# Performance work log

Hardware: AMD Instinct MI355X
Metric: run time of the kernel (lower is better)

Reference implementation:

```python
import jax, jax.numpy as jnp
import numpy as np

B, N, CI, CP, H, W, R = 2, 8192, 64, 64, 128, 128, 4
D = (CI + CP) // R  # qk channels = 32
BN_EPS = 1e-5


def setup_inputs() -> dict:
    key = jax.random.key(0)
    ks = jax.random.split(key, 8)
    pts_img = jax.random.uniform(ks[0], (B, N, 2), minval=-1.0, maxval=1.0)
    img_feats = jax.random.normal(ks[1], (B, CI, H, W), dtype=jnp.float32)
    pts_feats = jax.random.normal(ks[2], (B, CP, N), dtype=jnp.float32)
    qk_w = jax.random.normal(ks[3], (D, CI + CP), dtype=jnp.float32) * 0.05
    v_w = jax.random.normal(ks[4], (CP, CP), dtype=jnp.float32) * 0.05
    v_b = jnp.zeros((CP,), dtype=jnp.float32)
    t_w = jax.random.normal(ks[5], (CP, CP), dtype=jnp.float32) * 0.05
    t_b = jnp.zeros((CP,), dtype=jnp.float32)
    bn_gamma = jnp.ones((CP,), dtype=jnp.float32)
    bn_beta = jnp.zeros((CP,), dtype=jnp.float32)
    return dict(pts_img=pts_img, img_feats=img_feats, pts_feats=pts_feats,
                qk_w=qk_w, v_w=v_w, v_b=v_b, t_w=t_w, t_b=t_b,
                bn_gamma=bn_gamma, bn_beta=bn_beta)


def _grid_sample(img_feats, pts_img):
    # torch.nn.functional.grid_sample: bilinear, zeros padding, align_corners=False
    # img_feats [B,C,H,W], pts_img [B,N,2] with (x,y) in [-1,1] -> [B,C,N]
    ix = (pts_img[..., 0] + 1.0) * 0.5 * W - 0.5
    iy = (pts_img[..., 1] + 1.0) * 0.5 * H - 0.5
    x0 = jnp.floor(ix); y0 = jnp.floor(iy)
    x1 = x0 + 1.0;      y1 = y0 + 1.0
    wx1 = ix - x0; wx0 = 1.0 - wx1
    wy1 = iy - y0; wy0 = 1.0 - wy1

    def gather(imgb, yi, xi):  # imgb [C,H,W]; yi,xi [N] float corner coords
        valid = ((xi >= 0) & (xi <= W - 1) & (yi >= 0) & (yi <= H - 1)).astype(imgb.dtype)
        xc = jnp.clip(xi, 0, W - 1).astype(jnp.int32)
        yc = jnp.clip(yi, 0, H - 1).astype(jnp.int32)
        return imgb[:, yc, xc] * valid  # [C,N], zeros outside

    def per_batch(imgb, x0, x1, y0, y1, wx0, wx1, wy0, wy1):
        return (gather(imgb, y0, x0) * (wy0 * wx0) + gather(imgb, y0, x1) * (wy0 * wx1)
                + gather(imgb, y1, x0) * (wy1 * wx0) + gather(imgb, y1, x1) * (wy1 * wx1))

    return jax.vmap(per_batch)(img_feats, x0, x1, y0, y1, wx0, wx1, wy0, wy1)


def reference(pts_img, img_feats, pts_feats, qk_w, v_w, v_b, t_w, t_b, bn_gamma, bn_beta):
    # grid-sample image features at point projections, concat with point features
    pts_wise_img = _grid_sample(img_feats, pts_img)                 # [B,CI,N]
    fusion = jnp.concatenate([pts_wise_img, pts_feats], axis=1)     # [B,CI+CP,N]

    # shared-weight 1x1 conv Q/K (bias=False), V with bias
    x_q = jnp.einsum('dc,bcn->bnd', qk_w, fusion)                   # [B,N,D]
    x_k = jnp.einsum('dc,bcn->bdn', qk_w, fusion)                   # [B,D,N]
    x_v = jnp.einsum('oc,bcn->bon', v_w, pts_feats) + v_b[None, :, None]  # [B,CP,N]

    energy = jnp.einsum('bnd,bdm->bnm', x_q, x_k)                   # [B,N,N]
    attention = jax.nn.softmax(energy, axis=-1)
    # L1 renormalization over rows (dim=1): divide each column by its column-sum
    attention = attention / (1e-9 + attention.sum(axis=1, keepdims=True))

    x_r = jnp.einsum('bcn,bnm->bcm', x_v, attention)                # [B,CP,N]

    # trans_conv(pts_feats - x_r) -> BatchNorm1d (training stats) -> ReLU
    y = jnp.einsum('oc,bcn->bon', t_w, pts_feats - x_r) + t_b[None, :, None]
    mean = y.mean(axis=(0, 2), keepdims=True)
    var = y.var(axis=(0, 2), keepdims=True)  # biased, matching torch BN
    y = (y - mean) * jax.lax.rsqrt(var + BN_EPS)
    y = y * bn_gamma[None, :, None] + bn_beta[None, :, None]
    x_r_out = jax.nn.relu(y)

    return pts_feats + x_r_out
```

## Files before the change

### kernel.cpp

```cpp
#include <hip/hip_runtime.h>
#include <math.h>

#define BB 2
#define NN 8192
#define CI 64
#define CP 64
#define HH 128
#define WW 128
#define DD 32
#define CF 128
#define SPLITM 8
#define SPLITN 4

typedef __bf16 bf16_t;
typedef __bf16 bf16x8 __attribute__((ext_vector_type(8)));
typedef __bf16 bf16x4 __attribute__((ext_vector_type(4)));
typedef float f32x4 __attribute__((ext_vector_type(4)));

#define SQ_L2E 1.2011224087864498f

__device__ __forceinline__ float fexp2(float x) { return __builtin_amdgcn_exp2f(x); }

__device__ __forceinline__ bf16x8 pack8(float a0,float a1,float a2,float a3,
                                        float b0,float b1,float b2,float b3){
    bf16x8 r;
    r[0]=(bf16_t)a0; r[1]=(bf16_t)a1; r[2]=(bf16_t)a2; r[3]=(bf16_t)a3;
    r[4]=(bf16_t)b0; r[5]=(bf16_t)b1; r[6]=(bf16_t)b2; r[7]=(bf16_t)b3;
    return r;
}

__device__ __forceinline__ bf16x8 ld_av(const bf16_t* p){
    bf16x4 lo = *(const bf16x4*)p;
    bf16x4 hi = *(const bf16x4*)(p + 16);
    bf16x8 r;
    r[0]=lo[0];r[1]=lo[1];r[2]=lo[2];r[3]=lo[3];
    r[4]=hi[0];r[5]=hi[1];r[6]=hi[2];r[7]=hi[3];
    return r;
}

__device__ __forceinline__ void gload_lds16(const void* g, void* l) {
    __builtin_amdgcn_global_load_lds(
        (const __attribute__((address_space(1))) unsigned int*)g,
        (__attribute__((address_space(3))) unsigned int*)l, 16, 0, 0);
}

__global__ __launch_bounds__(256) void k_timg(const float* __restrict__ img, float* __restrict__ imgT) {
    __shared__ float tile[64][65];
    int b = blockIdx.y;
    int pos0 = blockIdx.x * 64;
    int tid = threadIdx.x;
    int q = tid >> 6, r = tid & 63;
    const float* src = img + (size_t)b * CI * (HH * WW);
#pragma unroll
    for (int cc = 0; cc < 16; ++cc) {
        int c = cc * 4 + q;
        tile[c][r] = src[(size_t)c * (HH * WW) + pos0 + r];
    }
    __syncthreads();
    float* dst = imgT + ((size_t)b * (HH * WW) + pos0) * 64;
#pragma unroll
    for (int pp = 0; pp < 16; ++pp) {
        int pos = pp * 4 + q;
        dst[(size_t)pos * 64 + r] = tile[r][pos];
    }
}

__global__ __launch_bounds__(256) void k_fuse(
    const float* __restrict__ pts_img, const float* __restrict__ imgT,
    const float* __restrict__ pfeat, const float* __restrict__ qkw,
    const float* __restrict__ vw, const float* __restrict__ vb,
    bf16_t* __restrict__ Qb, bf16_t* __restrict__ XVb)
{
    __shared__ __align__(16) float qk_l[DD * 132];
    __shared__ __align__(16) float vw_l[CP * 68];
    __shared__ __align__(16) float fus[16][CF];
    __shared__ bf16_t xvout[64][20];
    int tid = threadIdx.x;
    for (int i = tid; i < DD * CF; i += 256) qk_l[(i >> 7) * 132 + (i & 127)] = qkw[i];
    for (int i = tid; i < CP * CP; i += 256) vw_l[(i >> 6) * 68 + (i & 63)] = vw[i];

    int w = tid >> 6, l = tid & 63;
    int p0 = blockIdx.x * 16;
    int bb = p0 / NN, n0 = p0 % NN;

#pragma unroll
    for (int i = 0; i < 4; ++i) {
        int pt = i * 4 + w;
        int n = n0 + pt;
        float x = pts_img[(size_t)(p0 + pt) * 2 + 0];
        float y = pts_img[(size_t)(p0 + pt) * 2 + 1];
        float ix = (x + 1.f) * 0.5f * WW - 0.5f;
        float iy = (y + 1.f) * 0.5f * HH - 0.5f;
        float x0 = floorf(ix), y0 = floorf(iy);
        float wx1 = ix - x0, wx0 = 1.f - wx1;
        float wy1 = iy - y0, wy0 = 1.f - wy1;
        int xi0 = (int)x0, yi0 = (int)y0;
        const float* base = imgT + (size_t)bb * (HH * WW) * 64 + l;
        float iv = 0.f;
#pragma unroll
        for (int cr = 0; cr < 4; ++cr) {
            int xi = xi0 + (cr & 1), yi = yi0 + (cr >> 1);
            float wgt = ((cr & 1) ? wx1 : wx0) * ((cr >> 1) ? wy1 : wy0);
            bool v = (xi >= 0) & (xi <= WW - 1) & (yi >= 0) & (yi <= HH - 1);
            int cx = min(max(xi, 0), WW - 1), cy = min(max(yi, 0), HH - 1);
            float s = base[((size_t)cy * WW + cx) * 64];
            iv += (v ? s : 0.f) * wgt;
        }
        float pv = pfeat[((size_t)bb * CP + l) * NN + n];
        fus[pt][l] = iv;
        fus[pt][64 + l] = pv;
    }
    __syncthreads();
#pragma unroll
    for (int i = 0; i < 4; ++i) {
        int pt = i * 4 + w;
        int n = n0 + pt;
        {
            int qo = l & 31, kh = l >> 5;
            const float4* qr = (const float4*)&qk_l[qo * 132 + kh * 64];
            const float4* fp = (const float4*)&fus[pt][kh * 64];
            float acc = 0.f;
#pragma unroll
            for (int k = 0; k < 16; ++k) {
                float4 a = qr[k], bq = fp[k];
                acc += a.x * bq.x + a.y * bq.y + a.z * bq.z + a.w * bq.w;
            }
            acc += __shfl_xor(acc, 32);
            if (kh == 0) Qb[((size_t)bb * NN + n) * DD + qo] = (bf16_t)(acc * SQ_L2E);
        }
        {
            const float4* vr = (const float4*)&vw_l[l * 68];
            const float4* fp = (const float4*)&fus[pt][64];
            float acc = vb[l];
#pragma unroll
            for (int k = 0; k < 16; ++k) {
                float4 a = vr[k], bv = fp[k];
                acc += a.x * bv.x + a.y * bv.y + a.z * bv.z + a.w * bv.w;
            }
            xvout[l][pt] = (bf16_t)acc;
        }
    }
    __syncthreads();
    {
        int c = tid >> 2, seg = (tid & 3) * 4;
        bf16x4 vv;
        vv[0] = xvout[c][seg + 0];
        vv[1] = xvout[c][seg + 1];
        vv[2] = xvout[c][seg + 2];
        vv[3] = xvout[c][seg + 3];
        *(bf16x4*)&XVb[((size_t)bb * CP + c) * NN + n0 + seg] = vv;
    }
}

__global__ __launch_bounds__(256) void k_rowsum(
    const bf16_t* __restrict__ Qb, float* __restrict__ rowsumG)
{
    int b = blockIdx.z;
    int n0 = blockIdx.x * 64;
    int mchunk = blockIdx.y * (NN / SPLITM);
    int tid = threadIdx.x;
    int wv = tid >> 6, l = tid & 63;
    int g = l >> 4, c16 = l & 15;
    const bf16x8* Qv = (const bf16x8*)(Qb + (size_t)b * NN * DD);
    f32x4 z = {0.f, 0.f, 0.f, 0.f};

    bf16x8 A0 = Qv[(size_t)(n0 +  0 + c16) * 4 + g];
    bf16x8 A1 = Qv[(size_t)(n0 + 16 + c16) * 4 + g];
    bf16x8 A2 = Qv[(size_t)(n0 + 32 + c16) * 4 + g];
    bf16x8 A3 = Qv[(size_t)(n0 + 48 + c16) * 4 + g];

    float rs[4][4];
#pragma unroll
    for (int a = 0; a < 4; ++a)
#pragma unroll
        for (int r = 0; r < 4; ++r) rs[a][r] = 0.f;

    int mbase = mchunk + wv * 64;
    bf16x8 Bn0 = Qv[(size_t)(mbase +  0 + c16) * 4 + g];
    bf16x8 Bn1 = Qv[(size_t)(mbase + 16 + c16) * 4 + g];
    bf16x8 Bn2 = Qv[(size_t)(mbase + 32 + c16) * 4 + g];
    bf16x8 Bn3 = Qv[(size_t)(mbase + 48 + c16) * 4 + g];

    const int NIT = NN / SPLITM / 256;
    for (int it = 0; it < NIT; ++it) {
        bf16x8 B0 = Bn0, B1 = Bn1, B2 = Bn2, B3 = Bn3;
        int mnext = mbase + 256;
        if (it + 1 < NIT) {
            Bn0 = Qv[(size_t)(mnext +  0 + c16) * 4 + g];
            Bn1 = Qv[(size_t)(mnext + 16 + c16) * 4 + g];
            Bn2 = Qv[(size_t)(mnext + 32 + c16) * 4 + g];
            Bn3 = Qv[(size_t)(mnext + 48 + c16) * 4 + g];
        }
#define ROWSTEP(Aa, a)                                                        \
        {                                                                     \
            f32x4 e0 = __builtin_amdgcn_mfma_f32_16x16x32_bf16(Aa, B0, z, 0, 0, 0); \
            f32x4 e1 = __builtin_amdgcn_mfma_f32_16x16x32_bf16(Aa, B1, z, 0, 0, 0); \
            f32x4 e2 = __builtin_amdgcn_mfma_f32_16x16x32_bf16(Aa, B2, z, 0, 0, 0); \
            f32x4 e3 = __builtin_amdgcn_mfma_f32_16x16x32_bf16(Aa, B3, z, 0, 0, 0); \
            _Pragma("unroll")                                                 \
            for (int r = 0; r < 4; ++r)                                       \
                rs[a][r] += (fexp2(e0[r]) + fexp2(e1[r])) + (fexp2(e2[r]) + fexp2(e3[r])); \
        }
        ROWSTEP(A0, 0) ROWSTEP(A1, 1) ROWSTEP(A2, 2) ROWSTEP(A3, 3)
#undef ROWSTEP
        mbase = mnext;
    }
#pragma unroll
    for (int a = 0; a < 4; ++a)
#pragma unroll
        for (int r = 0; r < 4; ++r) {
            float v = rs[a][r];
            v += __shfl_xor(v, 1);
            v += __shfl_xor(v, 2);
            v += __shfl_xor(v, 4);
            v += __shfl_xor(v, 8);
            if (c16 == 0)
                atomicAdd(&rowsumG[(size_t)b * NN + n0 + 16 * a + 4 * g + r], v);
        }
}

__global__ __launch_bounds__(256) void k_scale(
    const float* __restrict__ rowsumG, const bf16_t* __restrict__ XVb,
    bf16_t* __restrict__ XVs, bf16_t* __restrict__ irsb)
{
    int b = blockIdx.y;
    int cq = blockIdx.z;
    int n = (blockIdx.x * 256 + threadIdx.x) * 4;
    float4 rs = *(const float4*)&rowsumG[(size_t)b * NN + n];
    float ir0 = 1.f / rs.x, ir1 = 1.f / rs.y, ir2 = 1.f / rs.z, ir3 = 1.f / rs.w;
    if (cq == 0) {
        bf16x4 iv;
        iv[0] = (bf16_t)ir0; iv[1] = (bf16_t)ir1; iv[2] = (bf16_t)ir2; iv[3] = (bf16_t)ir3;
        *(bf16x4*)&irsb[(size_t)b * NN + n] = iv;
    }
    const bf16_t* src = XVb + ((size_t)b * CP + cq * 16) * NN + n;
    char* dstbase = (char*)(XVs + ((size_t)b * CP + cq * 16) * NN);
    size_t nb = (size_t)n * 2;
    size_t hi = nb & ~(size_t)255;
    size_t lo = nb & 255;
#pragma unroll
    for (int c = 0; c < 16; ++c) {
        bf16x4 v = *(const bf16x4*)&src[(size_t)c * NN];
        bf16x4 o;
        o[0] = (bf16_t)((float)v[0] * ir0);
        o[1] = (bf16_t)((float)v[1] * ir1);
        o[2] = (bf16_t)((float)v[2] * ir2);
        o[3] = (bf16_t)((float)v[3] * ir3);
        size_t sb = hi | (lo ^ ((size_t)(c & 7) << 4));
        *(bf16x4*)(dstbase + (size_t)c * NN * 2 + sb) = o;
    }
}

__device__ __forceinline__ void stage_tile(const char* xvbase, int n0, char* ldsbuf, int wv, int l) {
#pragma unroll
    for (int k = 0; k < 2; ++k) {
        int R0 = k * 32 + wv * 4;
        int row = R0 + (l >> 4);
        const char* g = xvbase + (size_t)row * (NN * 2) + (size_t)n0 * 2 + (size_t)(l & 15) * 16;
        gload_lds16(g, ldsbuf + R0 * 256);
    }
}

__global__ __launch_bounds__(512, 4) void k_attn(
    const bf16_t* __restrict__ Qb, const bf16_t* __restrict__ XVs,
    const bf16_t* __restrict__ irsb,
    bf16_t* __restrict__ part, float* __restrict__ cpart)
{
    __shared__ __align__(16) char lds[4 * 64 * 72 * 2];
    __shared__ float csL[4 * 64];

    int b = blockIdx.z;
    int m0 = blockIdx.x * 64;
    int chunk = blockIdx.y;
    int tid = threadIdx.x;
    int wv = tid >> 6, l = tid & 63;
    int g = l >> 4, c16 = l & 15;
    int q4 = wv & 3;
    int jh = wv >> 2;

    const bf16x8* Qv = (const bf16x8*)(Qb + (size_t)b * NN * DD);
    const char* xvbase = (const char*)(XVs + (size_t)b * CP * NN);
    const bf16_t* irow = irsb + (size_t)b * NN;

    bf16x8 bqA = Qv[(size_t)(m0 + jh * 32 + c16) * 4 + g];
    bf16x8 bqB = Qv[(size_t)(m0 + jh * 32 + 16 + c16) * 4 + g];

    f32x4 z = {0.f, 0.f, 0.f, 0.f};
    f32x4 acc[4][2];
    f32x4 acsA = z, acsB = z;
#pragma unroll
    for (int ci = 0; ci < 4; ++ci) { acc[ci][0] = z; acc[ci][1] = z; }

    const int NT = (NN / SPLITN) / 128;
    int nbase = chunk * (NN / SPLITN);

    stage_tile(xvbase, nbase, lds, wv, l);
    int nwin = nbase + q4 * 32;
    bf16x8 a0 = Qv[(size_t)(nwin + c16) * 4 + g];
    bf16x8 a1 = Qv[(size_t)(nwin + 16 + c16) * 4 + g];
    bf16x8 cif = ld_av(irow + nwin + 4 * g);
    __syncthreads();

    const int swz = (c16 & 7) << 4;
    const int blo = (q4 * 32 + 4 * g) * 2;
    const int lo_off = blo ^ swz;
    const int hi_off = (blo + 32) ^ swz;

    for (int t = 0; t < NT; ++t) {
        char* buf = lds + (t & 1) * 16384;
        if (t + 1 < NT)
            stage_tile(xvbase, nbase + (t + 1) * 128, lds + ((t + 1) & 1) * 16384, wv, l);

        bf16x8 ca0 = a0, ca1 = a1, cf = cif;

        f32x4 EA0 = __builtin_amdgcn_mfma_f32_16x16x32_bf16(ca0, bqA, z, 0, 0, 0);
        f32x4 EA1 = __builtin_amdgcn_mfma_f32_16x16x32_bf16(ca1, bqA, z, 0, 0, 0);
        f32x4 EB0 = __builtin_amdgcn_mfma_f32_16x16x32_bf16(ca0, bqB, z, 0, 0, 0);
        f32x4 EB1 = __builtin_amdgcn_mfma_f32_16x16x32_bf16(ca1, bqB, z, 0, 0, 0);

        bf16x8 bpA = pack8(fexp2(EA0[0]), fexp2(EA0[1]), fexp2(EA0[2]), fexp2(EA0[3]),
                           fexp2(EA1[0]), fexp2(EA1[1]), fexp2(EA1[2]), fexp2(EA1[3]));
        bf16x8 bpB = pack8(fexp2(EB0[0]), fexp2(EB0[1]), fexp2(EB0[2]), fexp2(EB0[3]),
                           fexp2(EB1[0]), fexp2(EB1[1]), fexp2(EB1[2]), fexp2(EB1[3]));

        acsA = __builtin_amdgcn_mfma_f32_16x16x32_bf16(cf, bpA, acsA, 0, 0, 0);
        acsB = __builtin_amdgcn_mfma_f32_16x16x32_bf16(cf, bpB, acsB, 0, 0, 0);

#pragma unroll
        for (int ci = 0; ci < 4; ++ci) {
            const char* rp = buf + (16 * ci + c16) * 256;
            bf16x4 lo = *(const bf16x4*)(rp + lo_off);
            bf16x4 hi = *(const bf16x4*)(rp + hi_off);
            bf16x8 xv;
            xv[0]=lo[0];xv[1]=lo[1];xv[2]=lo[2];xv[3]=lo[3];
            xv[4]=hi[0];xv[5]=hi[1];xv[6]=hi[2];xv[7]=hi[3];
            acc[ci][0] = __builtin_amdgcn_mfma_f32_16x16x32_bf16(xv, bpA, acc[ci][0], 0, 0, 0);
            acc[ci][1] = __builtin_amdgcn_mfma_f32_16x16x32_bf16(xv, bpB, acc[ci][1], 0, 0, 0);
        }

        if (t + 1 < NT) {
            int nw2 = nbase + (t + 1) * 128 + q4 * 32;
            a0 = Qv[(size_t)(nw2 + c16) * 4 + g];
            a1 = Qv[(size_t)(nw2 + 16 + c16) * 4 + g];
            cif = ld_av(irow + nw2 + 4 * g);
        }
        __syncthreads();
    }

    if (l < 16) {
        csL[q4 * 64 + 16 * (2 * jh + 0) + l] = acsA[0];
        csL[q4 * 64 + 16 * (2 * jh + 1) + l] = acsB[0];
    }
    bf16_t* epi = (bf16_t*)lds;
#pragma unroll
    for (int ci = 0; ci < 4; ++ci)
#pragma unroll
        for (int jj = 0; jj < 2; ++jj)
#pragma unroll
            for (int r = 0; r < 4; ++r) {
                int cc = 16 * ci + 4 * g + r;
                int mm = jh * 32 + jj * 16 + c16;
                epi[((size_t)q4 * 64 + cc) * 72 + mm] = (bf16_t)acc[ci][jj][r];
            }
    __syncthreads();
    {
        int c = tid >> 3, m8 = (tid & 7) * 8;
        float s[8] = {0.f,0.f,0.f,0.f,0.f,0.f,0.f,0.f};
#pragma unroll
        for (int q = 0; q < 4; ++q) {
            bf16x8 v = *(const bf16x8*)&epi[((size_t)q * 64 + c) * 72 + m8];
#pragma unroll
            for (int i = 0; i < 8; ++i) s[i] += (float)v[i];
        }
        bf16x8 o;
#pragma unroll
        for (int i = 0; i < 8; ++i) o[i] = (bf16_t)s[i];
        *(bf16x8*)&part[(((size_t)chunk * BB + b) * CP + c) * NN + m0 + m8] = o;
    }
    if (tid < 64) {
        float cp = csL[tid] + csL[64 + tid] + csL[128 + tid] + csL[192 + tid];
        cpart[((size_t)chunk * BB + b) * NN + m0 + tid] = cp;
    }
}

__global__ __launch_bounds__(256) void k_post(
    const bf16_t* __restrict__ part, const float* __restrict__ cpart,
    const float* __restrict__ pfeat, const float* __restrict__ tw,
    const float* __restrict__ tb, float* __restrict__ Y)
{
    __shared__ float Tl[64][66];
    __shared__ float twt[64][68];
    int tid = threadIdx.x;
    int b = blockIdx.y;
    int n0 = blockIdx.x * 64;
    int nl = tid & 63;
    int grp = tid >> 6;

    for (int i = tid; i < 64 * 64; i += 256)
        twt[i & 63][i >> 6] = tw[i];

    float cs = 0.f;
#pragma unroll
    for (int sp = 0; sp < SPLITN; ++sp)
        cs += cpart[((size_t)sp * BB + b) * NN + n0 + nl];
    float ic = 1.f / (1e-9f + cs);
#pragma unroll
    for (int k = 0; k < 16; ++k) {
        int c = k * 4 + grp;
        float xr = 0.f;
#pragma unroll
        for (int sp = 0; sp < SPLITN; ++sp)
            xr += (float)part[(((size_t)sp * BB + b) * CP + c) * NN + n0 + nl];
        Tl[c][nl] = pfeat[((size_t)b * CP + c) * NN + n0 + nl] - xr * ic;
    }
    __syncthreads();

    float y0 = tb[grp * 16 + 0], y1 = tb[grp * 16 + 1], y2 = tb[grp * 16 + 2], y3 = tb[grp * 16 + 3];
    float y4 = tb[grp * 16 + 4], y5 = tb[grp * 16 + 5], y6 = tb[grp * 16 + 6], y7 = tb[grp * 16 + 7];
    float y8 = tb[grp * 16 + 8], y9 = tb[grp * 16 + 9], yA = tb[grp * 16 +10], yB = tb[grp * 16 +11];
    float yC = tb[grp * 16 +12], yD = tb[grp * 16 +13], yE = tb[grp * 16 +14], yF = tb[grp * 16 +15];
#pragma unroll 4
    for (int c = 0; c < 64; ++c) {
        float t = Tl[c][nl];
        const float4* wr = (const float4*)&twt[c][grp * 16];
        float4 w0 = wr[0], w1 = wr[1], w2 = wr[2], w3 = wr[3];
        y0 += w0.x * t; y1 += w0.y * t; y2 += w0.z * t; y3 += w0.w * t;
        y4 += w1.x * t; y5 += w1.y * t; y6 += w1.z * t; y7 += w1.w * t;
        y8 += w2.x * t; y9 += w2.y * t; yA += w2.z * t; yB += w2.w * t;
        yC += w3.x * t; yD += w3.y * t; yE += w3.z * t; yF += w3.w * t;
    }
    float* yb = Y + ((size_t)b * CP + grp * 16) * NN + n0 + nl;
    yb[0 * NN] = y0;  yb[1 * NN] = y1;  yb[2 * NN] = y2;  yb[3 * NN] = y3;
    yb[4 * NN] = y4;  yb[5 * NN] = y5;  yb[6 * NN] = y6;  yb[7 * NN] = y7;
    yb[8 * NN] = y8;  yb[9 * NN] = y9;  yb[10 * NN] = yA; yb[11 * NN] = yB;
    yb[12 * NN] = yC; yb[13 * NN] = yD; yb[14 * NN] = yE; yb[15 * NN] = yF;
}

__global__ __launch_bounds__(256) void k_bnstat(
    const float* __restrict__ Y, float* __restrict__ bnred)
{
    __shared__ float red[8];
    int tid = threadIdx.x;
    int o = blockIdx.y, b = blockIdx.z;
    const float* row = Y + ((size_t)b * CP + o) * NN + blockIdx.x * 2048 + tid * 8;
    float4 a = *(const float4*)row;
    float4 c4 = *(const float4*)(row + 4);
    float sv = ((a.x + a.y) + (a.z + a.w)) + ((c4.x + c4.y) + (c4.z + c4.w));
    float sq = ((a.x*a.x + a.y*a.y) + (a.z*a.z + a.w*a.w))
             + ((c4.x*c4.x + c4.y*c4.y) + (c4.z*c4.z + c4.w*c4.w));
#pragma unroll
    for (int off = 1; off < 64; off <<= 1) {
        sv += __shfl_xor(sv, off);
        sq += __shfl_xor(sq, off);
    }
    int wv = tid >> 6;
    if ((tid & 63) == 0) { red[wv] = sv; red[4 + wv] = sq; }
    __syncthreads();
    if (tid == 0) {
        atomicAdd(&bnred[o], red[0] + red[1] + red[2] + red[3]);
        atomicAdd(&bnred[64 + o], red[4] + red[5] + red[6] + red[7]);
    }
}

__global__ __launch_bounds__(256) void k_final(
    const float* __restrict__ Y, const float* __restrict__ pfeat,
    const float* __restrict__ gamma, const float* __restrict__ beta,
    const float* __restrict__ bnred, float* __restrict__ out)
{
    int idx4 = blockIdx.x * 256 + threadIdx.x;
    int o = ((idx4 * 4) / NN) & (CP - 1);
    const float invcnt = 1.f / (float)(BB * NN);
    float mean = bnred[o] * invcnt;
    float var = bnred[64 + o] * invcnt - mean * mean;
    float sc = gamma[o] * rsqrtf(var + 1e-5f);
    float sh = beta[o] - mean * sc;
    float4 y = ((const float4*)Y)[idx4];
    float4 p = ((const float4*)pfeat)[idx4];
    float4 r;
    r.x = p.x + fmaxf(y.x * sc + sh, 0.f);
    r.y = p.y + fmaxf(y.y * sc + sh, 0.f);
    r.z = p.z + fmaxf(y.z * sc + sh, 0.f);
    r.w = p.w + fmaxf(y.w * sc + sh, 0.f);
    ((float4*)out)[idx4] = r;
}

extern "C" void kernel_launch(void* const* d_in, const int* in_sizes, int n_in,
                              void* d_out, int out_size, void* d_ws, size_t ws_size,
                              hipStream_t stream) {
    const float* pts_img = (const float*)d_in[0];
    const float* img     = (const float*)d_in[1];
    const float* pfeat   = (const float*)d_in[2];
    const float* qkw     = (const float*)d_in[3];
    const float* vw      = (const float*)d_in[4];
    const float* vb      = (const float*)d_in[5];
    const float* tw      = (const float*)d_in[6];
    const float* tb      = (const float*)d_in[7];
    const float* gamma   = (const float*)d_in[8];
    const float* beta    = (const float*)d_in[9];

    char* base = (char*)d_ws;
    bf16_t* Qb      = (bf16_t*)(base);
    bf16_t* XVb     = (bf16_t*)(base + 1048576);
    bf16_t* XVs     = (bf16_t*)(base + 3145728);
    float*  rowsumG = (float*)(base + 5251072);
    float*  bn      = (float*)(base + 5316608);
    bf16_t* irsb    = (bf16_t*)(base + 5317120);
    float*  cpart   = (float*)(base + 5349888);
    float*  Y       = (float*)(base + 5874176);
    bf16_t* part    = (bf16_t*)(base + 10068480);
    float*  imgT    = (float*)(base + 26845696);

    hipMemsetAsync(base + 5251072, 0, 66048, stream);
    k_timg<<<dim3((HH * WW) / 64, BB), 256, 0, stream>>>(img, imgT);
    k_fuse<<<(BB * NN) / 16, 256, 0, stream>>>(pts_img, imgT, pfeat, qkw, vw, vb, Qb, XVb);
    k_rowsum<<<dim3(NN / 64, SPLITM, BB), 256, 0, stream>>>(Qb, rowsumG);
    k_scale<<<dim3(NN / 1024, BB, 4), 256, 0, stream>>>(rowsumG, XVb, XVs, irsb);
    k_attn<<<dim3(NN / 64, SPLITN, BB), 512, 0, stream>>>(Qb, XVs, irsb, part, cpart);
    k_post<<<dim3(NN / 64, BB), 256, 0, stream>>>(part, cpart, pfeat, tw, tb, Y);
    k_bnstat<<<dim3(NN / 2048, CP, BB), 256, 0, stream>>>(Y, bn);
    k_final<<<(BB * CP * NN) / 1024, 256, 0, stream>>>(Y, pfeat, gamma, beta, bn, (float*)d_out);
}
```

Measured before the change: 116.3 us.

## Software-pipeline energy MFMAs, halve attention split, fuse BN stats into post kernel

The attention loop now computes the next tile's QK energy MFMAs one iteration ahead, prefetches Q fragments two tiles ahead, and raises wave priority around the accumulation MFMAs, so exp and MFMA work overlap. SPLITN drops from 4 to 2, which halves the grid and the partial-sum traffic but gives each block a longer loop. The separate BN statistics kernel is removed; k_post now reduces sum and sum-of-squares with wave shuffles and atomics, saving one launch and a full read of Y. The cost is more atomics and fewer resident blocks for k_attn.

```diff
diff --git a/kernel.cpp b/kernel.cpp
--- a/kernel.cpp
+++ b/kernel.cpp
@@ -10,7 +10,7 @@
 #define DD 32
 #define CF 128
 #define SPLITM 8
-#define SPLITN 4
+#define SPLITN 2
 
 typedef __bf16 bf16_t;
 typedef __bf16 bf16x8 __attribute__((ext_vector_type(8)));
@@ -295,10 +295,20 @@
     int nbase = chunk * (NN / SPLITN);
 
     stage_tile(xvbase, nbase, lds, wv, l);
-    int nwin = nbase + q4 * 32;
-    bf16x8 a0 = Qv[(size_t)(nwin + c16) * 4 + g];
-    bf16x8 a1 = Qv[(size_t)(nwin + 16 + c16) * 4 + g];
-    bf16x8 cif = ld_av(irow + nwin + 4 * g);
+    int nw0 = nbase + q4 * 32;
+    bf16x8 aN0 = Qv[(size_t)(nw0 + c16) * 4 + g];
+    bf16x8 aN1 = Qv[(size_t)(nw0 + 16 + c16) * 4 + g];
+    bf16x8 cifC = ld_av(irow + nw0 + 4 * g);
+
+    f32x4 EA0 = __builtin_amdgcn_mfma_f32_16x16x32_bf16(aN0, bqA, z, 0, 0, 0);
+    f32x4 EA1 = __builtin_amdgcn_mfma_f32_16x16x32_bf16(aN1, bqA, z, 0, 0, 0);
+    f32x4 EB0 = __builtin_amdgcn_mfma_f32_16x16x32_bf16(aN0, bqB, z, 0, 0, 0);
+    f32x4 EB1 = __builtin_amdgcn_mfma_f32_16x16x32_bf16(aN1, bqB, z, 0, 0, 0);
+
+    int nw1 = nbase + 128 + q4 * 32;
+    aN0 = Qv[(size_t)(nw1 + c16) * 4 + g];
+    aN1 = Qv[(size_t)(nw1 + 16 + c16) * 4 + g];
+    bf16x8 cifN = ld_av(irow + nw1 + 4 * g);
     __syncthreads();
 
     const int swz = (c16 & 7) << 4;
@@ -311,21 +321,31 @@
         if (t + 1 < NT)
             stage_tile(xvbase, nbase + (t + 1) * 128, lds + ((t + 1) & 1) * 16384, wv, l);
 
-        bf16x8 ca0 = a0, ca1 = a1, cf = cif;
-
-        f32x4 EA0 = __builtin_amdgcn_mfma_f32_16x16x32_bf16(ca0, bqA, z, 0, 0, 0);
-        f32x4 EA1 = __builtin_amdgcn_mfma_f32_16x16x32_bf16(ca1, bqA, z, 0, 0, 0);
-        f32x4 EB0 = __builtin_amdgcn_mfma_f32_16x16x32_bf16(ca0, bqB, z, 0, 0, 0);
-        f32x4 EB1 = __builtin_amdgcn_mfma_f32_16x16x32_bf16(ca1, bqB, z, 0, 0, 0);
-
         bf16x8 bpA = pack8(fexp2(EA0[0]), fexp2(EA0[1]), fexp2(EA0[2]), fexp2(EA0[3]),
                            fexp2(EA1[0]), fexp2(EA1[1]), fexp2(EA1[2]), fexp2(EA1[3]));
         bf16x8 bpB = pack8(fexp2(EB0[0]), fexp2(EB0[1]), fexp2(EB0[2]), fexp2(EB0[3]),
                            fexp2(EB1[0]), fexp2(EB1[1]), fexp2(EB1[2]), fexp2(EB1[3]));
 
-        acsA = __builtin_amdgcn_mfma_f32_16x16x32_bf16(cf, bpA, acsA, 0, 0, 0);
-        acsB = __builtin_amdgcn_mfma_f32_16x16x32_bf16(cf, bpB, acsB, 0, 0, 0);
-
+        if (t + 1 < NT) {
+            EA0 = __builtin_amdgcn_mfma_f32_16x16x32_bf16(aN0, bqA, z, 0, 0, 0);
+            EA1 = __builtin_amdgcn_mfma_f32_16x16x32_bf16(aN1, bqA, z, 0, 0, 0);
+            EB0 = __builtin_amdgcn_mfma_f32_16x16x32_bf16(aN0, bqB, z, 0, 0, 0);
+            EB1 = __builtin_amdgcn_mfma_f32_16x16x32_bf16(aN1, bqB, z, 0, 0, 0);
+        }
+        bf16x8 cifU = cifC;
+        if (t + 2 < NT) {
+            int nw2 = nbase + (t + 2) * 128 + q4 * 32;
+            aN0 = Qv[(size_t)(nw2 + c16) * 4 + g];
+            aN1 = Qv[(size_t)(nw2 + 16 + c16) * 4 + g];
+            cifC = cifN;
+            cifN = ld_av(irow + nw2 + 4 * g);
+        } else {
+            cifC = cifN;
+        }
+
+        __builtin_amdgcn_s_setprio(1);
+        acsA = __builtin_amdgcn_mfma_f32_16x16x32_bf16(cifU, bpA, acsA, 0, 0, 0);
+        acsB = __builtin_amdgcn_mfma_f32_16x16x32_bf16(cifU, bpB, acsB, 0, 0, 0);
 #pragma unroll
         for (int ci = 0; ci < 4; ++ci) {
             const char* rp = buf + (16 * ci + c16) * 256;
@@ -337,13 +357,7 @@
             acc[ci][0] = __builtin_amdgcn_mfma_f32_16x16x32_bf16(xv, bpA, acc[ci][0], 0, 0, 0);
             acc[ci][1] = __builtin_amdgcn_mfma_f32_16x16x32_bf16(xv, bpB, acc[ci][1], 0, 0, 0);
         }
-
-        if (t + 1 < NT) {
-            int nw2 = nbase + (t + 1) * 128 + q4 * 32;
-            a0 = Qv[(size_t)(nw2 + c16) * 4 + g];
-            a1 = Qv[(size_t)(nw2 + 16 + c16) * 4 + g];
-            cif = ld_av(irow + nw2 + 4 * g);
-        }
+        __builtin_amdgcn_s_setprio(0);
         __syncthreads();
     }
 
@@ -386,7 +400,7 @@
 __global__ __launch_bounds__(256) void k_post(
     const bf16_t* __restrict__ part, const float* __restrict__ cpart,
     const float* __restrict__ pfeat, const float* __restrict__ tw,
-    const float* __restrict__ tb, float* __restrict__ Y)
+    const float* __restrict__ tb, float* __restrict__ Y, float* __restrict__ bnred)
 {
     __shared__ float Tl[64][66];
     __shared__ float twt[64][68];
@@ -434,32 +448,26 @@
     yb[4 * NN] = y4;  yb[5 * NN] = y5;  yb[6 * NN] = y6;  yb[7 * NN] = y7;
     yb[8 * NN] = y8;  yb[9 * NN] = y9;  yb[10 * NN] = yA; yb[11 * NN] = yB;
     yb[12 * NN] = yC; yb[13 * NN] = yD; yb[14 * NN] = yE; yb[15 * NN] = yF;
-}
-
-__global__ __launch_bounds__(256) void k_bnstat(
-    const float* __restrict__ Y, float* __restrict__ bnred)
-{
-    __shared__ float red[8];
-    int tid = threadIdx.x;
-    int o = blockIdx.y, b = blockIdx.z;
-    const float* row = Y + ((size_t)b * CP + o) * NN + blockIdx.x * 2048 + tid * 8;
-    float4 a = *(const float4*)row;
-    float4 c4 = *(const float4*)(row + 4);
-    float sv = ((a.x + a.y) + (a.z + a.w)) + ((c4.x + c4.y) + (c4.z + c4.w));
-    float sq = ((a.x*a.x + a.y*a.y) + (a.z*a.z + a.w*a.w))
-             + ((c4.x*c4.x + c4.y*c4.y) + (c4.z*c4.z + c4.w*c4.w));
-#pragma unroll
-    for (int off = 1; off < 64; off <<= 1) {
-        sv += __shfl_xor(sv, off);
-        sq += __shfl_xor(sq, off);
-    }
-    int wv = tid >> 6;
-    if ((tid & 63) == 0) { red[wv] = sv; red[4 + wv] = sq; }
-    __syncthreads();
-    if (tid == 0) {
-        atomicAdd(&bnred[o], red[0] + red[1] + red[2] + red[3]);
-        atomicAdd(&bnred[64 + o], red[4] + red[5] + red[6] + red[7]);
-    }
+
+#define BNRED(YV, OI)                                                          \
+    {                                                                          \
+        float sv = YV, sq = YV * YV;                                           \
+        sv += __shfl_xor(sv, 1);  sq += __shfl_xor(sq, 1);                     \
+        sv += __shfl_xor(sv, 2);  sq += __shfl_xor(sq, 2);                     \
+        sv += __shfl_xor(sv, 4);  sq += __shfl_xor(sq, 4);                     \
+        sv += __shfl_xor(sv, 8);  sq += __shfl_xor(sq, 8);                     \
+        sv += __shfl_xor(sv, 16); sq += __shfl_xor(sq, 16);                    \
+        sv += __shfl_xor(sv, 32); sq += __shfl_xor(sq, 32);                    \
+        if (nl == 0) {                                                         \
+            atomicAdd(&bnred[grp * 16 + OI], sv);                              \
+            atomicAdd(&bnred[64 + grp * 16 + OI], sq);                         \
+        }                                                                      \
+    }
+    BNRED(y0, 0)  BNRED(y1, 1)  BNRED(y2, 2)  BNRED(y3, 3)
+    BNRED(y4, 4)  BNRED(y5, 5)  BNRED(y6, 6)  BNRED(y7, 7)
+    BNRED(y8, 8)  BNRED(y9, 9)  BNRED(yA, 10) BNRED(yB, 11)
+    BNRED(yC, 12) BNRED(yD, 13) BNRED(yE, 14) BNRED(yF, 15)
+#undef BNRED
 }
 
 __global__ __launch_bounds__(256) void k_final(
@@ -516,7 +524,6 @@
     k_rowsum<<<dim3(NN / 64, SPLITM, BB), 256, 0, stream>>>(Qb, rowsumG);
     k_scale<<<dim3(NN / 1024, BB, 4), 256, 0, stream>>>(rowsumG, XVb, XVs, irsb);
     k_attn<<<dim3(NN / 64, SPLITN, BB), 512, 0, stream>>>(Qb, XVs, irsb, part, cpart);
-    k_post<<<dim3(NN / 64, BB), 256, 0, stream>>>(part, cpart, pfeat, tw, tb, Y);
-    k_bnstat<<<dim3(NN / 2048, CP, BB), 256, 0, stream>>>(Y, bn);
+    k_post<<<dim3(NN / 64, BB), 256, 0, stream>>>(part, cpart, pfeat, tw, tb, Y, bn);
     k_final<<<(BB * CP * NN) / 1024, 256, 0, stream>>>(Y, pfeat, gamma, beta, bn, (float*)d_out);
 }
```

After: 210.4 us. 80.9% more time.
